# Kernel optimization log

Measured on AMD Instinct MI355X. Metric: run time of the kernel, lower is better.

The kernel has to match this reference:

```python
import jax, jax.numpy as jnp
import numpy as np

EMBED_DIM = 1024
NUM_HEADS = 16
HEAD_DIM = EMBED_DIM // NUM_HEADS
SEQ = 2048
BSZ = 2


def setup_inputs() -> dict:
    key = jax.random.key(0)
    ks = jax.random.split(key, 12)
    f = jnp.float32
    query = jax.random.normal(ks[0], (SEQ, BSZ, EMBED_DIM), f)
    k_in = jax.random.normal(ks[1], (SEQ, BSZ, EMBED_DIM), f)
    v_in = jax.random.normal(ks[2], (SEQ, BSZ, EMBED_DIM), f)
    s = 0.02  # weight init scale
    q_w = jax.random.normal(ks[3], (EMBED_DIM, EMBED_DIM), f) * s
    q_b = jax.random.normal(ks[4], (EMBED_DIM,), f) * s
    k_w = jax.random.normal(ks[5], (EMBED_DIM, EMBED_DIM), f) * s
    k_b = jax.random.normal(ks[6], (EMBED_DIM,), f) * s
    v_w = jax.random.normal(ks[7], (EMBED_DIM, EMBED_DIM), f) * s
    v_b = jax.random.normal(ks[8], (EMBED_DIM,), f) * s
    o_w_mean = jax.random.normal(ks[9], (EMBED_DIM, EMBED_DIM), f) * s
    # lgstd ~ uniform(2*log(stdv), log(stdv)) with stdv = 1/sqrt(out+1)
    stdv = 1.0 / np.sqrt(EMBED_DIM + 1)
    o_w_lgstd = jax.random.uniform(ks[10], (EMBED_DIM, EMBED_DIM), f,
                                   2.0 * np.log(stdv), np.log(stdv))
    eps = jax.random.normal(ks[11], (EMBED_DIM, EMBED_DIM), f) * 1.5  # N(0, 1.5)
    return dict(query=query, key=k_in, value=v_in,
                q_w=q_w, q_b=q_b, k_w=k_w, k_b=k_b, v_w=v_w, v_b=v_b,
                o_w_mean=o_w_mean, o_w_lgstd=o_w_lgstd, eps=eps)


def reference(query, key, value, q_w, q_b, k_w, k_b, v_w, v_b,
              o_w_mean, o_w_lgstd, eps):
    tgt_len, bsz, embed_dim = query.shape
    scaling = HEAD_DIM ** -0.5
    # projections (F.linear: x @ W.T + b)
    q = (query @ q_w.T + q_b) * scaling          # [S,B,E]
    k = key @ k_w.T + k_b                        # [S,B,E]
    v = value @ v_w.T + v_b                      # [S,B,E]
    # [S,B,E] -> [B*H, S, hd]
    def split_heads(x, L):
        return x.reshape(L, bsz * NUM_HEADS, HEAD_DIM).transpose(1, 0, 2)
    q = split_heads(q, tgt_len)
    k = split_heads(k, key.shape[0])
    v = split_heads(v, value.shape[0])
    src_len = k.shape[1]
    scores = jnp.einsum('bqd,bkd->bqk', q, k)    # [B*H, S, S] (explicit O(n^2))
    attn = jax.nn.softmax(scores, axis=-1)
    ctx = jnp.einsum('bqk,bkd->bqd', attn, v)    # [B*H, S, hd]
    ctx = ctx.transpose(1, 0, 2).reshape(tgt_len, bsz, embed_dim)
    # Bayesian output projection: sampled weight (training mode), no bias
    o_w = o_w_mean + eps * jnp.exp(o_w_lgstd)
    out = ctx @ o_w.T                            # [S,B,E]
    avg_attn = attn.reshape(bsz, NUM_HEADS, tgt_len, src_len).sum(axis=1) / NUM_HEADS
    return out, avg_attn
```

## Files before the change

### kernel.cpp

```cpp
#include <hip/hip_runtime.h>

#define SQ 2048
#define BB 2
#define EE 1024
#define HH 16
#define DD 64
#define MM (SQ*BB)
#define NSLICE 4
#define KSLICE (SQ/NSLICE)
#define KT_IN (KSLICE/128)
#define LOG2E 1.44269504f

typedef _Float16 f16;
typedef _Float16 half8 __attribute__((ext_vector_type(8)));
typedef _Float16 half4 __attribute__((ext_vector_type(4)));
typedef float f32x4 __attribute__((ext_vector_type(4)));

static __device__ __forceinline__ f32x4 mfma16(half8 a, half8 b, f32x4 c) {
    return __builtin_amdgcn_mfma_f32_16x16x32_f16(a, b, c, 0, 0, 0);
}

static __device__ __forceinline__ void gload16(const f16* g, f16* l) {
    __builtin_amdgcn_global_load_lds(
        (const __attribute__((address_space(1))) unsigned int*)g,
        (__attribute__((address_space(3))) unsigned int*)l, 16, 0, 0);
}

__global__ void k_elem(const float* __restrict__ q_w, const float* __restrict__ k_w,
                       const float* __restrict__ v_w, const float* __restrict__ query,
                       const float* __restrict__ key, const float* __restrict__ value,
                       const float* __restrict__ owm, const float* __restrict__ owl,
                       const float* __restrict__ eps,
                       f16* qw16, f16* kw16, f16* vw16,
                       f16* xq16, f16* xk16, f16* xv16, f16* ow16)
{
    int y = blockIdx.y;
    size_t i = ((size_t)blockIdx.x * 256 + threadIdx.x) * 4;
    if (y < 3) {
        if (i >= (size_t)EE*EE) return;
        const float* s = (y==0) ? q_w : (y==1) ? k_w : v_w;
        f16* d = (y==0) ? qw16 : (y==1) ? kw16 : vw16;
        float4 v = *(const float4*)&s[i];
        half4 o = {(f16)v.x, (f16)v.y, (f16)v.z, (f16)v.w};
        *(half4*)&d[i] = o;
    } else if (y < 6) {
        const float* s = (y==3) ? query : (y==4) ? key : value;
        f16* d = (y==3) ? xq16 : (y==4) ? xk16 : xv16;
        float4 v = *(const float4*)&s[i];
        half4 o = {(f16)v.x, (f16)v.y, (f16)v.z, (f16)v.w};
        *(half4*)&d[i] = o;
    } else {
        if (i >= (size_t)EE*EE) return;
        float4 m = *(const float4*)&owm[i];
        float4 l = *(const float4*)&owl[i];
        float4 e = *(const float4*)&eps[i];
        half4 o = {(f16)(m.x + e.x * __expf(l.x)), (f16)(m.y + e.y * __expf(l.y)),
                   (f16)(m.z + e.z * __expf(l.z)), (f16)(m.w + e.w * __expf(l.w))};
        *(half4*)&ow16[i] = o;
    }
}

__device__ __forceinline__ void gemm_body(
    const f16* __restrict__ A, const f16* __restrict__ W,
    const float* __restrict__ bias, float scale, void* __restrict__ out, int mode)
{
    __shared__ f16 As[128*32];
    __shared__ f16 Bs[64*32];
    int t = threadIdx.x, lane = t & 63, w = t >> 6;
    int quad = lane >> 4, m16 = lane & 15;
    int wm = w >> 1, wn = w & 1;
    int gm0 = blockIdx.x * 128, gn0 = blockIdx.y * 64;
    int arow = lane >> 2, apch = lane & 3;
    f32x4 acc[4][2] = {};
    for (int kt = 0; kt < EE; kt += 32) {
        #pragma unroll
        for (int j = 0; j < 2; ++j) {
            int row = w*32 + j*16 + arow;
            int lch = apch ^ (row & 3);
            gload16(&A[(size_t)(gm0+row)*EE + kt + lch*8], &As[row*32 + apch*8]);
        }
        {
            int row = w*16 + arow;
            int lch = apch ^ (row & 3);
            gload16(&W[(size_t)(gn0+row)*EE + kt + lch*8], &Bs[row*32 + apch*8]);
        }
        __syncthreads();
        int cs = (quad ^ (m16 & 3)) * 8;
        half8 af[4], bf[2];
        #pragma unroll
        for (int i = 0; i < 4; ++i) af[i] = *(half8*)&As[(wm*64 + i*16 + m16)*32 + cs];
        #pragma unroll
        for (int j = 0; j < 2; ++j) bf[j] = *(half8*)&Bs[(wn*32 + j*16 + m16)*32 + cs];
        #pragma unroll
        for (int i = 0; i < 4; ++i)
            #pragma unroll
            for (int j = 0; j < 2; ++j)
                acc[i][j] = mfma16(af[i], bf[j], acc[i][j]);
        __syncthreads();
    }
    #pragma unroll
    for (int j = 0; j < 2; ++j) {
        int col = gn0 + wn*32 + j*16 + m16;
        float bb = bias ? bias[col] : 0.0f;
        #pragma unroll
        for (int i = 0; i < 4; ++i) {
            int r0 = gm0 + wm*64 + i*16 + quad*4;
            #pragma unroll
            for (int r = 0; r < 4; ++r) {
                float v = (acc[i][j][r] + bb) * scale;
                int m = r0 + r;
                if (mode == 2)      ((float*)out)[(size_t)m*EE + col] = v;
                else if (mode == 1) ((f16*)out)[((size_t)(m & 1)*EE + col)*SQ + (m >> 1)] = (f16)v;
                else                ((f16*)out)[(size_t)m*EE + col] = (f16)v;
            }
        }
    }
}

__global__ __launch_bounds__(256) void k_gemm_qkv(
    const f16* xq, const f16* qw, const float* qb,
    const f16* xk, const f16* kw, const float* kb,
    const f16* xv, const f16* vw, const float* vb,
    f16* Q16, f16* K16, f16* Vt16)
{
    int z = blockIdx.z;
    const f16* A = (z==0) ? xq : (z==1) ? xk : xv;
    const f16* W = (z==0) ? qw : (z==1) ? kw : vw;
    const float* bi = (z==0) ? qb : (z==1) ? kb : vb;
    float sc = (z==0) ? 0.125f * LOG2E : 1.0f;
    void* o = (z==0) ? (void*)Q16 : (z==1) ? (void*)K16 : (void*)Vt16;
    gemm_body(A, W, bi, sc, o, (z==2) ? 1 : 0);
}

__global__ __launch_bounds__(256) void k_gemm_o(const f16* A, const f16* W, float* out)
{
    gemm_body(A, W, nullptr, 1.0f, out, 2);
}

__global__ __launch_bounds__(256, 4) void k_attn_l(
    const f16* __restrict__ Q16, const f16* __restrict__ K16, float* __restrict__ lse2)
{
    __shared__ float red[4][64];
    const int t = threadIdx.x, lane = t & 63, w = t >> 6;
    const int quad = lane >> 4, m16 = lane & 15;
    const int q0 = blockIdx.x * 64, h = blockIdx.y, b = blockIdx.z;

    half8 bq[4][2];
    #pragma unroll
    for (int nt = 0; nt < 4; ++nt)
        #pragma unroll
        for (int dk = 0; dk < 2; ++dk)
            bq[nt][dk] = *(const half8*)&Q16[(size_t)((q0 + nt*16 + m16)*BB + b)*EE + h*DD + dk*32 + quad*8];

    float lsum[4] = {};
    for (int kt = 0; kt < 16; ++kt) {
        half8 ak[2][2];
        #pragma unroll
        for (int mt = 0; mt < 2; ++mt)
            #pragma unroll
            for (int dk = 0; dk < 2; ++dk)
                ak[mt][dk] = *(const half8*)&K16[(size_t)((kt*128 + w*32 + mt*16 + m16)*BB + b)*EE + h*DD + dk*32 + quad*8];
        #pragma unroll
        for (int mt = 0; mt < 2; ++mt)
            #pragma unroll
            for (int nt = 0; nt < 4; ++nt) {
                f32x4 s = {};
                s = mfma16(ak[mt][0], bq[nt][0], s);
                s = mfma16(ak[mt][1], bq[nt][1], s);
                lsum[nt] += __builtin_amdgcn_exp2f(s[0]) + __builtin_amdgcn_exp2f(s[1])
                          + __builtin_amdgcn_exp2f(s[2]) + __builtin_amdgcn_exp2f(s[3]);
            }
    }
    #pragma unroll
    for (int nt = 0; nt < 4; ++nt) {
        float v = lsum[nt];
        v += __shfl_xor(v, 16, 64);
        v += __shfl_xor(v, 32, 64);
        lsum[nt] = v;
    }
    if (quad == 0)
        #pragma unroll
        for (int nt = 0; nt < 4; ++nt) red[w][nt*16 + m16] = lsum[nt];
    __syncthreads();
    if (t < 64) {
        float v = red[0][t] + red[1][t] + red[2][t] + red[3][t];
        lse2[((size_t)b*HH + h)*SQ + q0 + t] = __log2f(v);
    }
}

__global__ __launch_bounds__(256, 2) void k_attn_main(
    const f16* __restrict__ Q16, const f16* __restrict__ K16, const f16* __restrict__ Vt16,
    const float* __restrict__ lse2, float* __restrict__ ctxp, float* __restrict__ avg_out)
{
    __shared__ f16 ps[2][32][136];
    __shared__ float csh[HH][32];
    const int t = threadIdx.x, lane = t & 63, w = t >> 6;
    const int quad = lane >> 4, m16 = lane & 15;
    const int q0 = blockIdx.x * 32, sl = blockIdx.y, b = blockIdx.z;
    const int ks0 = sl * KSLICE;

    for (int i = t; i < HH*32; i += 256) {
        int hh = i >> 5, qq = i & 31;
        csh[hh][qq] = lse2[((size_t)b*HH + hh)*SQ + q0 + qq];
    }
    __syncthreads();

    float avg_r[KT_IN][16] = {};

    for (int hp = 0; hp < 8; ++hp) {
        f32x4 acc[2][2] = {};
        for (int hh2 = 0; hh2 < 2; ++hh2) {
            const int h = hp*2 + hh2;
            half8 bq[2][2];
            #pragma unroll
            for (int nt = 0; nt < 2; ++nt)
                #pragma unroll
                for (int dk = 0; dk < 2; ++dk)
                    bq[nt][dk] = *(const half8*)&Q16[(size_t)((q0 + nt*16 + m16)*BB + b)*EE + h*DD + dk*32 + quad*8];
            const float c01[2] = { csh[h][m16], csh[h][16 + m16] };

            half8 ak[2][2][2], bv[2][4];
            #pragma unroll
            for (int mt = 0; mt < 2; ++mt)
                #pragma unroll
                for (int dk = 0; dk < 2; ++dk)
                    ak[0][mt][dk] = *(const half8*)&K16[(size_t)((ks0 + w*32 + mt*16 + m16)*BB + b)*EE + h*DD + dk*32 + quad*8];
            #pragma unroll
            for (int ks = 0; ks < 4; ++ks)
                bv[0][ks] = *(const half8*)&Vt16[((size_t)b*EE + h*DD + w*16 + m16)*SQ + ks0 + ks*32 + quad*8];

            #pragma unroll
            for (int kt = 0; kt < KT_IN; ++kt) {
                const int cur = kt & 1, nxt = cur ^ 1;
                if (kt + 1 < KT_IN) {
                    #pragma unroll
                    for (int mt = 0; mt < 2; ++mt)
                        #pragma unroll
                        for (int dk = 0; dk < 2; ++dk)
                            ak[nxt][mt][dk] = *(const half8*)&K16[(size_t)((ks0 + (kt+1)*128 + w*32 + mt*16 + m16)*BB + b)*EE + h*DD + dk*32 + quad*8];
                    #pragma unroll
                    for (int ks = 0; ks < 4; ++ks)
                        bv[nxt][ks] = *(const half8*)&Vt16[((size_t)b*EE + h*DD + w*16 + m16)*SQ + ks0 + (kt+1)*128 + ks*32 + quad*8];
                }
                #pragma unroll
                for (int mt = 0; mt < 2; ++mt)
                    #pragma unroll
                    for (int nt = 0; nt < 2; ++nt) {
                        f32x4 s = {};
                        s = mfma16(ak[cur][mt][0], bq[nt][0], s);
                        s = mfma16(ak[cur][mt][1], bq[nt][1], s);
                        half4 ph;
                        #pragma unroll
                        for (int r = 0; r < 4; ++r) {
                            float p = __builtin_amdgcn_exp2f(s[r] - c01[nt]);
                            avg_r[kt][mt*8 + nt*4 + r] += p;
                            ph[r] = (f16)p;
                        }
                        *(half4*)&ps[cur][nt*16 + m16][w*32 + mt*16 + quad*4] = ph;
                    }
                __syncthreads();
                #pragma unroll
                for (int qt = 0; qt < 2; ++qt) {
                    f32x4 c4 = acc[hh2][qt];
                    #pragma unroll
                    for (int ks = 0; ks < 4; ++ks) {
                        half8 ap = *(half8*)&ps[cur][qt*16 + m16][ks*32 + quad*8];
                        c4 = mfma16(ap, bv[cur][ks], c4);
                    }
                    acc[hh2][qt] = c4;
                }
            }
        }
        #pragma unroll
        for (int hh2 = 0; hh2 < 2; ++hh2)
            #pragma unroll
            for (int qt = 0; qt < 2; ++qt)
                #pragma unroll
                for (int r = 0; r < 4; ++r) {
                    int q = q0 + qt*16 + quad*4 + r;
                    ctxp[(size_t)sl*MM*EE + ((size_t)q*BB + b)*EE + (hp*2 + hh2)*DD + w*16 + m16] = acc[hh2][qt][r];
                }
    }
    #pragma unroll
    for (int kt = 0; kt < KT_IN; ++kt)
        #pragma unroll
        for (int mt = 0; mt < 2; ++mt)
            #pragma unroll
            for (int nt = 0; nt < 2; ++nt) {
                int q = q0 + nt*16 + m16;
                int k = ks0 + kt*128 + w*32 + mt*16 + quad*4;
                float4 v = { avg_r[kt][mt*8+nt*4+0]*(1.0f/HH), avg_r[kt][mt*8+nt*4+1]*(1.0f/HH),
                             avg_r[kt][mt*8+nt*4+2]*(1.0f/HH), avg_r[kt][mt*8+nt*4+3]*(1.0f/HH) };
                *(float4*)&avg_out[((size_t)b*SQ + q)*SQ + k] = v;
            }
}

__global__ void k_ctx_red(const float* __restrict__ ctxp, f16* __restrict__ ctx16) {
    size_t i = ((size_t)blockIdx.x * 256 + threadIdx.x) * 4;
    float4 s = *(const float4*)&ctxp[i];
    #pragma unroll
    for (int sl = 1; sl < NSLICE; ++sl) {
        float4 v = *(const float4*)&ctxp[(size_t)sl*MM*EE + i];
        s.x += v.x; s.y += v.y; s.z += v.z; s.w += v.w;
    }
    half4 o = {(f16)s.x, (f16)s.y, (f16)s.z, (f16)s.w};
    *(half4*)&ctx16[i] = o;
}

extern "C" void kernel_launch(void* const* d_in, const int* in_sizes, int n_in,
                              void* d_out, int out_size, void* d_ws, size_t ws_size,
                              hipStream_t stream) {
    const float* query    = (const float*)d_in[0];
    const float* key      = (const float*)d_in[1];
    const float* value    = (const float*)d_in[2];
    const float* q_w      = (const float*)d_in[3];
    const float* q_b      = (const float*)d_in[4];
    const float* k_w      = (const float*)d_in[5];
    const float* k_b      = (const float*)d_in[6];
    const float* v_w      = (const float*)d_in[7];
    const float* v_b      = (const float*)d_in[8];
    const float* o_w_mean = (const float*)d_in[9];
    const float* o_w_lgstd= (const float*)d_in[10];
    const float* eps      = (const float*)d_in[11];
    float* out = (float*)d_out;
    float* avg = out + (size_t)MM * EE;

    const size_t EWN = (size_t)EE*EE;
    const size_t XWN = (size_t)MM*EE;
    f16* qw16  = (f16*)d_ws;
    f16* kw16  = qw16 + EWN;
    f16* vw16  = kw16 + EWN;
    f16* ow16  = vw16 + EWN;
    f16* Q16   = ow16 + EWN;
    f16* K16   = Q16  + XWN;
    f16* Vt16  = K16  + XWN;
    f16* ctx16 = Vt16 + XWN;
    float* lse2 = (float*)(ctx16 + XWN);
    f16* xq16  = (f16*)(lse2 + (size_t)BB*HH*SQ);
    f16* xk16  = xq16 + XWN;
    f16* xv16  = xk16 + XWN;
    float* ctxp = (float*)xq16;

    k_elem<<<dim3(XWN/1024, 7), 256, 0, stream>>>(q_w, k_w, v_w, query, key, value,
        o_w_mean, o_w_lgstd, eps, qw16, kw16, vw16, xq16, xk16, xv16, ow16);

    k_gemm_qkv<<<dim3(MM/128, EE/64, 3), 256, 0, stream>>>(
        xq16, qw16, q_b, xk16, kw16, k_b, xv16, vw16, v_b, Q16, K16, Vt16);

    k_attn_l   <<<dim3(SQ/64, HH, BB), 256, 0, stream>>>(Q16, K16, lse2);
    k_attn_main<<<dim3(SQ/32, NSLICE, BB), 256, 0, stream>>>(Q16, K16, Vt16, lse2, ctxp, avg);
    k_ctx_red  <<<XWN/1024, 256, 0, stream>>>(ctxp, ctx16);

    k_gemm_o<<<dim3(MM/128, EE/64), 256, 0, stream>>>(ctx16, ow16, out);
}
```

Baseline: 400.4 us.

## Halve attention query tile to 16 rows and flatten head/key loop into pipelined rounds

The main attention kernel now processes 16 query rows per block instead of 32, doubling the grid and raising the launch bound to 4 blocks per CU to cut register pressure and raise occupancy. The head and key-tile loops are flattened into a single round sequence so the K prefetch crosses head boundaries, and Q is reloaded per head. V is no longer double-buffered and is loaded just before the barrier. Each K/V tile is now reloaded by twice as many blocks, doubling that global/L2 traffic, while per-block accumulator state shrinks.

After: 518.9 us. 29.6% more time.

```diff
diff --git a/kernel.cpp b/kernel.cpp
--- a/kernel.cpp
+++ b/kernel.cpp
@@ -188,111 +188,120 @@
     }
 }
 
-__global__ __launch_bounds__(256, 2) void k_attn_main(
+__global__ __launch_bounds__(256, 4) void k_attn_main(
     const f16* __restrict__ Q16, const f16* __restrict__ K16, const f16* __restrict__ Vt16,
     const float* __restrict__ lse2, float* __restrict__ ctxp, float* __restrict__ avg_out)
 {
-    __shared__ f16 ps[2][32][136];
-    __shared__ float csh[HH][32];
+    __shared__ f16 ps[2][16][136];
+    __shared__ float csh[HH][16];
     const int t = threadIdx.x, lane = t & 63, w = t >> 6;
     const int quad = lane >> 4, m16 = lane & 15;
-    const int q0 = blockIdx.x * 32, sl = blockIdx.y, b = blockIdx.z;
+    const int q0 = blockIdx.x * 16, sl = blockIdx.y, b = blockIdx.z;
     const int ks0 = sl * KSLICE;
 
-    for (int i = t; i < HH*32; i += 256) {
-        int hh = i >> 5, qq = i & 31;
+    {
+        int hh = t >> 4, qq = t & 15;
         csh[hh][qq] = lse2[((size_t)b*HH + hh)*SQ + q0 + qq];
     }
+
+    float avg_r[KT_IN][8] = {};
+
+    half8 ak[2][2][2], bq[2], bv[4];
+    #pragma unroll
+    for (int mt = 0; mt < 2; ++mt)
+        #pragma unroll
+        for (int dk = 0; dk < 2; ++dk)
+            ak[0][mt][dk] = *(const half8*)&K16[(size_t)((ks0 + w*32 + mt*16 + m16)*BB + b)*EE + dk*32 + quad*8];
+    #pragma unroll
+    for (int dk = 0; dk < 2; ++dk)
+        bq[dk] = *(const half8*)&Q16[(size_t)((q0 + m16)*BB + b)*EE + dk*32 + quad*8];
+
     __syncthreads();
 
-    float avg_r[KT_IN][16] = {};
-
-    for (int hp = 0; hp < 8; ++hp) {
-        f32x4 acc[2][2] = {};
-        for (int hh2 = 0; hh2 < 2; ++hh2) {
-            const int h = hp*2 + hh2;
-            half8 bq[2][2];
-            #pragma unroll
-            for (int nt = 0; nt < 2; ++nt)
-                #pragma unroll
-                for (int dk = 0; dk < 2; ++dk)
-                    bq[nt][dk] = *(const half8*)&Q16[(size_t)((q0 + nt*16 + m16)*BB + b)*EE + h*DD + dk*32 + quad*8];
-            const float c01[2] = { csh[h][m16], csh[h][16 + m16] };
-
-            half8 ak[2][2][2], bv[2][4];
-            #pragma unroll
-            for (int mt = 0; mt < 2; ++mt)
-                #pragma unroll
-                for (int dk = 0; dk < 2; ++dk)
-                    ak[0][mt][dk] = *(const half8*)&K16[(size_t)((ks0 + w*32 + mt*16 + m16)*BB + b)*EE + h*DD + dk*32 + quad*8];
-            #pragma unroll
-            for (int ks = 0; ks < 4; ++ks)
-                bv[0][ks] = *(const half8*)&Vt16[((size_t)b*EE + h*DD + w*16 + m16)*SQ + ks0 + ks*32 + quad*8];
-
-            #pragma unroll
-            for (int kt = 0; kt < KT_IN; ++kt) {
-                const int cur = kt & 1, nxt = cur ^ 1;
-                if (kt + 1 < KT_IN) {
-                    #pragma unroll
-                    for (int mt = 0; mt < 2; ++mt)
-                        #pragma unroll
-                        for (int dk = 0; dk < 2; ++dk)
-                            ak[nxt][mt][dk] = *(const half8*)&K16[(size_t)((ks0 + (kt+1)*128 + w*32 + mt*16 + m16)*BB + b)*EE + h*DD + dk*32 + quad*8];
-                    #pragma unroll
-                    for (int ks = 0; ks < 4; ++ks)
-                        bv[nxt][ks] = *(const half8*)&Vt16[((size_t)b*EE + h*DD + w*16 + m16)*SQ + ks0 + (kt+1)*128 + ks*32 + quad*8];
-                }
+    f32x4 acc[2] = {};
+
+    for (int rp = 0; rp < 8; ++rp) {
+        #pragma unroll
+        for (int ri = 0; ri < 8; ++ri) {
+            const int round = rp*8 + ri;
+            const int h  = rp*2 + (ri >> 2);
+            const int kt = ri & 3;
+            const int cur = ri & 1, nxt = cur ^ 1;
+            const bool last = (rp == 7) && (ri == 7);
+
+            if (!last) {
+                const int rn  = round + 1;
+                const int hn  = rn >> 2, ktn = rn & 3;
                 #pragma unroll
                 for (int mt = 0; mt < 2; ++mt)
                     #pragma unroll
-                    for (int nt = 0; nt < 2; ++nt) {
-                        f32x4 s = {};
-                        s = mfma16(ak[cur][mt][0], bq[nt][0], s);
-                        s = mfma16(ak[cur][mt][1], bq[nt][1], s);
-                        half4 ph;
-                        #pragma unroll
-                        for (int r = 0; r < 4; ++r) {
-                            float p = __builtin_amdgcn_exp2f(s[r] - c01[nt]);
-                            avg_r[kt][mt*8 + nt*4 + r] += p;
-                            ph[r] = (f16)p;
-                        }
-                        *(half4*)&ps[cur][nt*16 + m16][w*32 + mt*16 + quad*4] = ph;
+                    for (int dk = 0; dk < 2; ++dk)
+                        ak[nxt][mt][dk] = *(const half8*)&K16[(size_t)((ks0 + ktn*128 + w*32 + mt*16 + m16)*BB + b)*EE + hn*DD + dk*32 + quad*8];
+            }
+
+            const float c0 = csh[h][m16];
+            #pragma unroll
+            for (int mt = 0; mt < 2; ++mt) {
+                f32x4 s = {};
+                s = mfma16(ak[cur][mt][0], bq[0], s);
+                s = mfma16(ak[cur][mt][1], bq[1], s);
+                half4 ph;
+                #pragma unroll
+                for (int r = 0; r < 4; ++r) {
+                    float p = __builtin_amdgcn_exp2f(s[r] - c0);
+                    avg_r[kt][mt*4 + r] += p;
+                    ph[r] = (f16)p;
+                }
+                *(half4*)&ps[cur][m16][w*32 + mt*16 + quad*4] = ph;
+            }
+
+            #pragma unroll
+            for (int ks = 0; ks < 4; ++ks)
+                bv[ks] = *(const half8*)&Vt16[((size_t)b*EE + h*DD + w*16 + m16)*SQ + ks0 + kt*128 + ks*32 + quad*8];
+
+            if ((ri == 3 || ri == 7) && !last) {
+                const int hn = (round + 1) >> 2;
+                #pragma unroll
+                for (int dk = 0; dk < 2; ++dk)
+                    bq[dk] = *(const half8*)&Q16[(size_t)((q0 + m16)*BB + b)*EE + hn*DD + dk*32 + quad*8];
+            }
+
+            __syncthreads();
+
+            {
+                f32x4 c4 = acc[(ri >> 2) & 1];
+                #pragma unroll
+                for (int ks = 0; ks < 4; ++ks) {
+                    half8 ap = *(half8*)&ps[cur][m16][ks*32 + quad*8];
+                    c4 = mfma16(ap, bv[ks], c4);
+                }
+                acc[(ri >> 2) & 1] = c4;
+            }
+
+            if (ri == 7) {
+                #pragma unroll
+                for (int hh2 = 0; hh2 < 2; ++hh2) {
+                    #pragma unroll
+                    for (int r = 0; r < 4; ++r) {
+                        int q = q0 + quad*4 + r;
+                        ctxp[(size_t)sl*MM*EE + ((size_t)q*BB + b)*EE + (h - 1 + hh2)*DD + w*16 + m16] = acc[hh2][r];
                     }
-                __syncthreads();
-                #pragma unroll
-                for (int qt = 0; qt < 2; ++qt) {
-                    f32x4 c4 = acc[hh2][qt];
-                    #pragma unroll
-                    for (int ks = 0; ks < 4; ++ks) {
-                        half8 ap = *(half8*)&ps[cur][qt*16 + m16][ks*32 + quad*8];
-                        c4 = mfma16(ap, bv[cur][ks], c4);
-                    }
-                    acc[hh2][qt] = c4;
+                    acc[hh2] = (f32x4){};
                 }
             }
         }
-        #pragma unroll
-        for (int hh2 = 0; hh2 < 2; ++hh2)
-            #pragma unroll
-            for (int qt = 0; qt < 2; ++qt)
-                #pragma unroll
-                for (int r = 0; r < 4; ++r) {
-                    int q = q0 + qt*16 + quad*4 + r;
-                    ctxp[(size_t)sl*MM*EE + ((size_t)q*BB + b)*EE + (hp*2 + hh2)*DD + w*16 + m16] = acc[hh2][qt][r];
-                }
-    }
+    }
+
     #pragma unroll
     for (int kt = 0; kt < KT_IN; ++kt)
         #pragma unroll
-        for (int mt = 0; mt < 2; ++mt)
-            #pragma unroll
-            for (int nt = 0; nt < 2; ++nt) {
-                int q = q0 + nt*16 + m16;
-                int k = ks0 + kt*128 + w*32 + mt*16 + quad*4;
-                float4 v = { avg_r[kt][mt*8+nt*4+0]*(1.0f/HH), avg_r[kt][mt*8+nt*4+1]*(1.0f/HH),
-                             avg_r[kt][mt*8+nt*4+2]*(1.0f/HH), avg_r[kt][mt*8+nt*4+3]*(1.0f/HH) };
-                *(float4*)&avg_out[((size_t)b*SQ + q)*SQ + k] = v;
-            }
+        for (int mt = 0; mt < 2; ++mt) {
+            int q = q0 + m16;
+            int k = ks0 + kt*128 + w*32 + mt*16 + quad*4;
+            float4 v = { avg_r[kt][mt*4+0]*(1.0f/HH), avg_r[kt][mt*4+1]*(1.0f/HH),
+                         avg_r[kt][mt*4+2]*(1.0f/HH), avg_r[kt][mt*4+3]*(1.0f/HH) };
+            *(float4*)&avg_out[((size_t)b*SQ + q)*SQ + k] = v;
+        }
 }
 
 __global__ void k_ctx_red(const float* __restrict__ ctxp, f16* __restrict__ ctx16) {
@@ -348,7 +357,7 @@
         xq16, qw16, q_b, xk16, kw16, k_b, xv16, vw16, v_b, Q16, K16, Vt16);
 
     k_attn_l   <<<dim3(SQ/64, HH, BB), 256, 0, stream>>>(Q16, K16, lse2);
-    k_attn_main<<<dim3(SQ/32, NSLICE, BB), 256, 0, stream>>>(Q16, K16, Vt16, lse2, ctxp, avg);
+    k_attn_main<<<dim3(SQ/16, NSLICE, BB), 256, 0, stream>>>(Q16, K16, Vt16, lse2, ctxp, avg);
     k_ctx_red  <<<XWN/1024, 256, 0, stream>>>(ctxp, ctx16);
 
     k_gemm_o<<<dim3(MM/128, EE/64), 256, 0, stream>>>(ctx16, ow16, out);
```
